# Performance work log

Measured on AMD Instinct MI355X. Metric: run time of the kernel, lower is better.

The kernel has to match this reference:

```python
import jax, jax.numpy as jnp
import numpy as np

NUM_LEVELS = 4
RADIUS = 4
H, W = 64, 128


def _bilinear_sample(feat, x, y):
    # feat: [N, Hl, Wl]; x, y: [N, K, K] pixel coords; zeros padding, align_corners=True
    N, Hl, Wl = feat.shape
    x0 = jnp.floor(x)
    y0 = jnp.floor(y)
    x1 = x0 + 1.0
    y1 = y0 + 1.0
    wx1 = x - x0
    wx0 = 1.0 - wx1
    wy1 = y - y0
    wy0 = 1.0 - wy1
    n_idx = jnp.arange(N)[:, None, None]

    def gather(xi, yi):
        inb = (xi >= 0) & (xi <= Wl - 1) & (yi >= 0) & (yi <= Hl - 1)
        xc = jnp.clip(xi, 0, Wl - 1).astype(jnp.int32)
        yc = jnp.clip(yi, 0, Hl - 1).astype(jnp.int32)
        v = feat[n_idx, yc, xc]
        return jnp.where(inb, v, jnp.zeros((), feat.dtype))

    return (gather(x0, y0) * wx0 * wy0 + gather(x1, y0) * wx1 * wy0
            + gather(x0, y1) * wx0 * wy1 + gather(x1, y1) * wx1 * wy1)


def _correlation(fmap1, fmap2, coords):
    bs, dim, h, w = fmap1.shape
    f1 = fmap1.reshape(bs, dim, h * w)
    f2 = fmap2.reshape(bs, dim, h * w)
    cv = jnp.einsum('bdm,bdn->bmn', f1, f2) / jnp.sqrt(jnp.asarray(dim, jnp.float32))
    cv = cv.reshape(bs * h * w, h, w)
    pyramid = [cv]
    for _ in range(NUM_LEVELS - 1):
        N, hl, wl = cv.shape
        cv = cv.reshape(N, hl // 2, 2, wl // 2, 2).mean(axis=(2, 4))  # avg_pool2d(2,2)
        pyramid.append(cv)

    cxy = coords.transpose(0, 2, 3, 1).astype(jnp.float32)  # [bs,h,w,2]
    cx = cxy[..., 0].reshape(-1)  # [bs*h*w]
    cy = cxy[..., 1].reshape(-1)
    r = RADIUS
    d = jnp.linspace(-r, r, 2 * r + 1, dtype=jnp.float32)
    dy, dx = jnp.meshgrid(d, d, indexing='ij')  # [K,K]

    outs = []
    for i, corr in enumerate(pyramid):
        scale = jnp.float32(2 ** i)
        x = cx[:, None, None] / scale + dx[None]
        y = cy[:, None, None] / scale + dy[None]
        sampled = _bilinear_sample(corr, x, y)  # [bs*h*w, K, K]
        outs.append(sampled.reshape(bs, h, w, -1))
    out = jnp.concatenate(outs, axis=-1)  # [bs,h,w,num_levels*K*K]
    return out.transpose(0, 3, 1, 2)


def setup_inputs() -> dict:
    key = jax.random.key(0)
    k1, k2, k3, k4 = jax.random.split(key, 4)
    fmap1 = jax.random.normal(k1, (1, 256, H, W), dtype=jnp.float32)
    fmap2 = jax.random.normal(k2, (1, 256, H, W), dtype=jnp.float32)
    cx = jax.random.uniform(k3, (1, 1, H, W), dtype=jnp.float32) * (W - 1)
    cy = jax.random.uniform(k4, (1, 1, H, W), dtype=jnp.float32) * (H - 1)
    coords = jnp.concatenate([cx, cy], axis=1)  # [1,2,H,W], channel 0 = x, 1 = y
    return {"fmap1": fmap1, "fmap2": fmap2, "coords": coords}


def reference(fmap1, fmap2, coords):
    return _correlation(fmap1, fmap2, coords)
```

## Files before the change

kernel.cpp:

```cpp
#include <hip/hip_runtime.h>
#include <stdint.h>

typedef _Float16 f16;
typedef __attribute__((ext_vector_type(8))) _Float16 f16x8;
typedef __attribute__((ext_vector_type(4))) float f32x4;
typedef __attribute__((ext_vector_type(2))) float fv2;
typedef __attribute__((ext_vector_type(4))) float fv4;

#define H0 64
#define W0 128
#define NPIX 8192
#define KD 256
#define NCAT 10880
#define OFF1 8192
#define OFF2 10240
#define OFF3 10752
#define CAP0 640
#define CAP1 2048
#define PL1OFF (32 * CAP0)
#define PLTOT (PL1OFF + 8 * CAP1)
#define ZTOT (64 + PLTOT + 64)


__global__ __launch_bounds__(256) void fused_pre(const float* __restrict__ in0,
                                                 const float* __restrict__ in1,
                                                 const float* __restrict__ coords,
                                                 f16* __restrict__ At,
                                                 f16* __restrict__ Bt,
                                                 int2* __restrict__ meta,
                                                 int* __restrict__ cnt) {
  __shared__ f16 tile[64][65];
  __shared__ int hist[40];
  __shared__ int base[40];
  int bid = blockIdx.x;
  int t = threadIdx.x;

  if (bid < 1024) {
    const float* in = (bid < 512) ? in0 : in1;
    f16* out = (bid < 512) ? At : Bt;
    size_t NR = (bid < 512) ? NPIX : NCAT;
    int bx = bid & 511;
    int m0 = (bx & 127) * 64;
    int d0 = (bx >> 7) * 64;
    int a = t & 63, b = t >> 6;
#pragma unroll
    for (int i = 0; i < 16; ++i) {
      int d = b + i * 4;
      tile[a][d] = (f16)in[(size_t)(d0 + d) * NPIX + m0 + a];
    }
    __syncthreads();
#pragma unroll
    for (int i = 0; i < 16; ++i) {
      int m = b + i * 4;
      int d = d0 + a;
      out[((size_t)(d >> 5) * NR + (m0 + m)) * 32 + (d & 31)] = tile[m][a];
    }
  } else if (bid < 1360) {
    int idx = (bid - 1024) * 256 + t;
    float acc[8] = {0, 0, 0, 0, 0, 0, 0, 0};
    int r, dc;
    if (idx < 65536) {
      int r1 = idx & 2047; dc = idx >> 11; r = r1;
      int y = r1 >> 6, x = r1 & 63;
#pragma unroll
      for (int e = 0; e < 8; ++e) {
        const float* p = in1 + (size_t)(dc * 8 + e) * NPIX + (y * 2) * W0 + x * 2;
        fv2 s0 = *(const fv2*)p;
        fv2 s1 = *(const fv2*)(p + W0);
        acc[e] = (s0[0] + s0[1] + s1[0] + s1[1]) * 0.25f;
      }
    } else if (idx < 81920) {
      int i2 = idx - 65536;
      int r2 = i2 & 511; dc = i2 >> 9; r = 2048 + r2;
      int y = r2 >> 5, x = r2 & 31;
#pragma unroll
      for (int e = 0; e < 8; ++e) {
        const float* p = in1 + (size_t)(dc * 8 + e) * NPIX + (y * 4) * W0 + x * 4;
        float s = 0.f;
#pragma unroll
        for (int h = 0; h < 4; ++h) {
          fv4 v = *(const fv4*)(p + h * W0);
          s += v[0] + v[1] + v[2] + v[3];
        }
        acc[e] = s * 0.0625f;
      }
    } else {
      int i3 = idx - 81920;
      int r3 = i3 & 127; dc = i3 >> 7; r = 2560 + r3;
      int y = r3 >> 4, x = r3 & 15;
#pragma unroll
      for (int e = 0; e < 8; ++e) {
        const float* p = in1 + (size_t)(dc * 8 + e) * NPIX + (y * 8) * W0 + x * 8;
        float s = 0.f;
#pragma unroll
        for (int h = 0; h < 8; ++h) {
          fv4 v0 = *(const fv4*)(p + h * W0);
          fv4 v1 = *(const fv4*)(p + h * W0 + 4);
          s += v0[0] + v0[1] + v0[2] + v0[3] + v1[0] + v1[1] + v1[2] + v1[3];
        }
        acc[e] = s * 0.015625f;
      }
    }
    f16x8 o;
#pragma unroll
    for (int e = 0; e < 8; ++e) o[e] = (f16)acc[e];
    *(f16x8*)(Bt + ((size_t)(dc >> 2) * NCAT + 8192 + r) * 32 + (dc & 3) * 8) = o;
  } else {
    int* plist = cnt + 64;
    int m = (bid - 1360) * 256 + t;
    if (t < 40) hist[t] = 0;
    __syncthreads();

    float cx = coords[m];
    float cy = coords[NPIX + m];
    int X0l[2], Y0l[2];
    int mx = 0, my = 0;
#pragma unroll
    for (int lev = 0; lev < 4; ++lev) {
      float inv = 1.0f / (float)(1 << lev);
      int X0 = (int)floorf(cx * inv) - 4;
      int Y0 = (int)floorf(cy * inv) - 4;
      if (lev < 2) { X0l[lev] = X0; Y0l[lev] = Y0; }
      mx |= (X0 & 0xff) << (8 * lev);
      my |= (Y0 & 0xff) << (8 * lev);
    }
    meta[m] = make_int2(mx, my);

    int b0 = (min(max(Y0l[0], 0), 63) >> 4) * 8 + (min(max(X0l[0], 0), 127) >> 4);
    int b1 = (min(max(Y0l[1], 0), 31) >> 4) * 4 + (min(max(X0l[1], 0), 63) >> 4);
    int s0 = atomicAdd(&hist[b0], 1);
    int s1 = atomicAdd(&hist[32 + b1], 1);
    __syncthreads();

    if (t < 40) base[t] = atomicAdd(&cnt[t], hist[t]);
    __syncthreads();

    int p0 = base[b0] + s0;
    if (p0 < CAP0) plist[b0 * CAP0 + p0] = m;
    int p1 = base[32 + b1] + s1;
    if (p1 < CAP1) plist[PL1OFF + b1 * CAP1 + p1] = m;
  }
}

__global__ __launch_bounds__(256, 2) void gemm_all(const f16* __restrict__ At,
                                                   const f16* __restrict__ Bt,
                                                   const int* __restrict__ cnt,
                                                   const int2* __restrict__ meta,
                                                   f16* __restrict__ Wbuf) {
  __shared__ f16 sa[8192];
  const int* plist = cnt + 64;
  int bid = blockIdx.x;
  int t = threadIdx.x;
  int lane = t & 63;
  int w = t >> 6;
  int lr = lane & 15;
  int ko = lane >> 4;

  if (bid < 160) {
    int bm = (((bid & 7) << 2) | ((bid >> 3) & 3)) << 8;
    int bn = OFF2 + ((bid >> 5) << 7);

    const f16* Ab = At + (size_t)(bm + w * 64 + lr) * 32 + ko * 8;
    const f16* Bb = Bt + (size_t)(bn + lr) * 32 + ko * 8;

    f16x8 af[2][4], bf[2][8];
#define LOADK(s, kk)                                                           \
    do {                                                                       \
      const f16* ap = Ab + (size_t)(kk) * (NPIX * 32);                         \
      const f16* bp = Bb + (size_t)(kk) * (NCAT * 32);                         \
      _Pragma("unroll")                                                        \
      for (int i = 0; i < 4; ++i) af[s][i] = *(const f16x8*)(ap + i * 512);    \
      _Pragma("unroll")                                                        \
      for (int i = 0; i < 8; ++i) bf[s][i] = *(const f16x8*)(bp + i * 512);    \
    } while (0)

    f32x4 acc[4][8];
#pragma unroll
    for (int i = 0; i < 4; ++i)
#pragma unroll
      for (int j = 0; j < 8; ++j) acc[i][j] = (f32x4){0.f, 0.f, 0.f, 0.f};

    LOADK(0, 0);
    LOADK(1, 1);
#pragma unroll
    for (int kk = 0; kk < 8; ++kk) {
      const int cur = kk & 1;
#pragma unroll
      for (int mi = 0; mi < 4; ++mi)
#pragma unroll
        for (int ni = 0; ni < 8; ++ni)
          acc[mi][ni] = __builtin_amdgcn_mfma_f32_16x16x32_f16(
              af[cur][mi], bf[cur][ni], acc[mi][ni], 0, 0, 0);
      if (kk + 2 < 8) LOADK(cur, kk + 2);
    }
#undef LOADK

    int lev, n0, wlog;
    if (bn < OFF3) { lev = 2; n0 = bn - OFF2; wlog = 5; }
    else           { lev = 3; n0 = bn - OFF3; wlog = 4; }
    int wmask = (1 << wlog) - 1;
    int yA = n0 >> wlog;
    int yB = (n0 + 127) >> wlog;
    int ycol[8], xcol[8];
#pragma unroll
    for (int ni = 0; ni < 8; ++ni) {
      int n = n0 + ni * 16 + lr;
      ycol[ni] = n >> wlog;
      xcol[ni] = n & wmask;
    }
    int sh = lev * 8;
#pragma unroll
    for (int mi = 0; mi < 4; ++mi)
#pragma unroll
      for (int r2 = 0; r2 < 4; ++r2) {
        int grow = bm + w * 64 + mi * 16 + ko * 4 + r2;
        int2 mv = meta[grow];
        int Y0 = (int)(signed char)((mv.y >> sh) & 0xff);
        if (Y0 <= yB && Y0 + 9 >= yA) {
          int X0 = (int)(signed char)((mv.x >> sh) & 0xff);
          f16* rowp = Wbuf + (size_t)grow * 512 + lev * 128;
#pragma unroll
          for (int ni = 0; ni < 8; ++ni) {
            int dy = ycol[ni] - Y0;
            int dx = xcol[ni] - X0;
            if ((unsigned)dy < 10u && (unsigned)dx < 10u)
              rowp[dy * 12 + dx] = (f16)(acc[mi][ni][r2] * 0.0625f);
          }
        }
      }
    return;
  }

  int bb = bid - 160;
  int lev, b, mg, half;
  if (bb < 1280) { lev = 0; b = bb / 40; int r = bb % 40; mg = r >> 1; half = r & 1; }
  else { lev = 1; int i = bb - 1280; b = i / 128; int r = i % 128; mg = r >> 1; half = r & 1; }

  int CAP   = lev ? CAP1 : CAP0;
  int cb    = min(cnt[lev ? 32 + b : b], CAP);
  if (mg * 32 >= cb) return;
  int Hl    = lev ? 32 : 64;
  int Wmap  = lev ? 64 : 128;
  int bx    = lev ? (b & 3) : (b & 7);
  int by    = lev ? (b >> 2) : (b >> 3);
  int x0 = bx * 16, y0 = by * 16;
  int NY = min(25, Hl - y0);
  int rowbase = lev ? 8192 : 0;
  int pbase = (lev ? PL1OFF + b * CAP1 : b * CAP0) + mg * 32;

  {
    int spix = t >> 3;
    int skk  = t & 7;
    int sp = plist[pbase + spix] & (NPIX - 1);
    const f16* g = At + (size_t)skk * (NPIX * 32) + (size_t)sp * 32;
    int line = spix >> 1;
    int sb = (spix & 1) * 4;
    f16* dst = sa + skk * 1024 + line * 64;
#pragma unroll
    for (int q = 0; q < 4; ++q) {
      int phys = (sb + q) ^ (line & 7) ^ skk;
      *(f16x8*)(dst + phys * 8) = *(const f16x8*)(g + q * 8);
    }
  }

  int aoff[2];
#pragma unroll
  for (int mi = 0; mi < 2; ++mi) {
    int pl = mi * 16 + lr;
    int line = pl >> 1;
    int phys = ((pl & 1) * 4 + ko) ^ (line & 7);
    aoff[mi] = line * 64 + phys * 8;
  }

  bool vst[4];
  int brow[4];
#pragma unroll
  for (int st = 0; st < 4; ++st) {
    int q = w + 4 * st;
    int yl = half * 13 + q;
    vst[st] = (q < (half ? 12 : 13)) && (yl < NY);
    int ylc = min(yl, NY - 1);
    brow[st] = rowbase + (y0 + ylc) * Wmap + x0 + lr;
  }

  f16x8 bf[2][8];
#define BLDB(s_, kk_)                                                          \
  do {                                                                         \
    const f16* bp = Bt + (size_t)(kk_) * (NCAT * 32) + ko * 8;                 \
    _Pragma("unroll")                                                          \
    for (int st = 0; st < 4; ++st) {                                           \
      bf[s_][st * 2]     = *(const f16x8*)(bp + (size_t)brow[st] * 32);        \
      bf[s_][st * 2 + 1] = *(const f16x8*)(bp + (size_t)(brow[st] + 16) * 32); \
    }                                                                          \
  } while (0)

  BLDB(0, 0);
  BLDB(1, 1);

  f32x4 acc[8][2];
#pragma unroll
  for (int i = 0; i < 8; ++i)
#pragma unroll
    for (int j = 0; j < 2; ++j) acc[i][j] = (f32x4){0.f, 0.f, 0.f, 0.f};

  __syncthreads();

#pragma unroll
  for (int kk = 0; kk < 8; ++kk) {
    const int cur = kk & 1;
    f16x8 a0 = *(const f16x8*)(sa + kk * 1024 + (aoff[0] ^ (kk * 8)));
    f16x8 a1 = *(const f16x8*)(sa + kk * 1024 + (aoff[1] ^ (kk * 8)));
#pragma unroll
    for (int nf = 0; nf < 8; ++nf) {
      acc[nf][0] = __builtin_amdgcn_mfma_f32_16x16x32_f16(a0, bf[cur][nf],
                                                          acc[nf][0], 0, 0, 0);
      acc[nf][1] = __builtin_amdgcn_mfma_f32_16x16x32_f16(a1, bf[cur][nf],
                                                          acc[nf][1], 0, 0, 0);
    }
    if (kk + 2 < 8) BLDB(cur, kk + 2);
  }
#undef BLDB

  int pe[2][4];
  int Xp[2][4], Yp[2][4];
  int sh = lev * 8;
#pragma unroll
  for (int mi = 0; mi < 2; ++mi)
#pragma unroll
    for (int r2 = 0; r2 < 4; ++r2) {
      int slot = mg * 32 + mi * 16 + ko * 4 + r2;
      int p = plist[pbase + mi * 16 + ko * 4 + r2] & (NPIX - 1);
      pe[mi][r2] = (slot < cb) ? p : -1;
      int2 mv = meta[p];
      Xp[mi][r2] = (int)(signed char)((mv.x >> sh) & 0xff);
      Yp[mi][r2] = (int)(signed char)((mv.y >> sh) & 0xff);
    }
#pragma unroll
  for (int st = 0; st < 4; ++st) {
    if (!vst[st]) continue;
    int y = y0 + half * 13 + w + 4 * st;
#pragma unroll
    for (int xc = 0; xc < 2; ++xc) {
      int x = x0 + xc * 16 + lr;
#pragma unroll
      for (int mi = 0; mi < 2; ++mi)
#pragma unroll
        for (int r2 = 0; r2 < 4; ++r2) {
          int p = pe[mi][r2];
          int dy = y - Yp[mi][r2];
          int dx = x - Xp[mi][r2];
          if (p >= 0 && (unsigned)dy < 10u && (unsigned)dx < 10u)
            Wbuf[(size_t)p * 512 + lev * 128 + dy * 12 + dx] =
                (f16)(acc[st * 2 + xc][mi][r2] * 0.0625f);
        }
    }
  }
}

__global__ __launch_bounds__(64) void corr_sample(const f16* __restrict__ Wbuf,
                                                  const float* __restrict__ coords,
                                                  float* __restrict__ out) {
  int tid = blockIdx.x * 64 + threadIdx.x;
  int m = tid & (NPIX - 1);
  int lev = tid >> 13;
  int Hl = H0 >> lev, Wl = W0 >> lev;

  float cx = coords[m];
  float cy = coords[NPIX + m];
  float inv = 1.0f / (float)(1 << lev);
  float xb = cx * inv, yb = cy * inv;
  float fx = floorf(xb), fy = floorf(yb);
  int X0 = (int)fx - 4, Y0 = (int)fy - 4;
  float wx1 = xb - fx, wx0 = 1.0f - wx1;
  float wy1 = yb - fy, wy0 = 1.0f - wy1;

  const f16* wb = Wbuf + (size_t)m * 512 + lev * 128;
  f16x8 rv[15];
#pragma unroll
  for (int i = 0; i < 15; ++i) rv[i] = *(const f16x8*)(wb + i * 8);

  float* op = out + (size_t)lev * 81 * NPIX + m;
  float cur[11], nxt[11];
#pragma unroll
  for (int i = 0; i < 11; ++i) {
    bool in = ((unsigned)Y0 < (unsigned)Hl) && ((unsigned)(X0 + i) < (unsigned)Wl);
    cur[i] = in ? (float)rv[i >> 3][i & 7] : 0.0f;
  }
#pragma unroll
  for (int j = 0; j < 9; ++j) {
    bool yin = (unsigned)(Y0 + j + 1) < (unsigned)Hl;
#pragma unroll
    for (int i = 0; i < 11; ++i) {
      int c = (j + 1) * 12 + i;
      bool in = yin && ((unsigned)(X0 + i) < (unsigned)Wl);
      nxt[i] = in ? (float)rv[c >> 3][c & 7] : 0.0f;
    }
#pragma unroll
    for (int i = 0; i < 9; ++i) {
      float v = wy0 * (wx0 * cur[i] + wx1 * cur[i + 1])
              + wy1 * (wx0 * nxt[i] + wx1 * nxt[i + 1]);
      op[(size_t)(j * 9 + i) * NPIX] = v;
    }
#pragma unroll
    for (int i = 0; i < 11; ++i) cur[i] = nxt[i];
  }
}

extern "C" void kernel_launch(void* const* d_in, const int* in_sizes, int n_in,
                              void* d_out, int out_size, void* d_ws, size_t ws_size,
                              hipStream_t stream) {
  const float* fmap1  = (const float*)d_in[0];
  const float* fmap2  = (const float*)d_in[1];
  const float* coords = (const float*)d_in[2];
  float* out = (float*)d_out;

  char* ws = (char*)d_ws;
  size_t offA = 0;
  size_t offB = offA + (size_t)NPIX * KD * 2;
  size_t offW = offB + (size_t)NCAT * KD * 2;
  size_t offM = offW + (size_t)NPIX * 512 * 2;
  size_t offC = offM + (size_t)NPIX * 8;
  size_t need = offC + (size_t)ZTOT * 4;
  if (ws_size < need) return;

  f16*  At   = (f16*)(ws + offA);
  f16*  Bt   = (f16*)(ws + offB);
  f16*  Wbuf = (f16*)(ws + offW);
  int2* meta = (int2*)(ws + offM);
  int*  cnt  = (int*)(ws + offC);

  hipMemsetAsync(cnt, 0, 64 * sizeof(int), stream);
  fused_pre<<<1392, 256, 0, stream>>>(fmap1, fmap2, coords, At, Bt, meta, cnt);
  gemm_all<<<2464, 256, 0, stream>>>(At, Bt, cnt, meta, Wbuf);
  corr_sample<<<512, 64, 0, stream>>>(Wbuf, coords, out);
}
```

Before: 74.71 us.

## Split gemm_all into single-wave blocks with finer pixel and tile-fragment partitioning

Converts gemm_all from 256-thread blocks to 64-thread single-wavefront blocks. The dense part now gets one block per former wave, and the sparse level-0/1 part gets one block per 16-pixel group × 8-fragment chunk. The A operand is loaded straight from global into registers instead of staged through shared memory, and the barrier is gone. The aim is better load balance and finer early-exit on sparse bins. In exchange the grid grows to many more tiny blocks, A is no longer reused across waves, and per-block launch and metadata overhead go up.

Result: slower. 85.20 us (+14.0%).

```diff
diff --git a/kernel.cpp b/kernel.cpp
--- a/kernel.cpp
+++ b/kernel.cpp
@@ -142,23 +142,22 @@
   }
 }
 
-__global__ __launch_bounds__(256, 2) void gemm_all(const f16* __restrict__ At,
-                                                   const f16* __restrict__ Bt,
-                                                   const int* __restrict__ cnt,
-                                                   const int2* __restrict__ meta,
-                                                   f16* __restrict__ Wbuf) {
-  __shared__ f16 sa[8192];
+__global__ __launch_bounds__(64) void gemm_all(const f16* __restrict__ At,
+                                               const f16* __restrict__ Bt,
+                                               const int* __restrict__ cnt,
+                                               const int2* __restrict__ meta,
+                                               f16* __restrict__ Wbuf) {
   const int* plist = cnt + 64;
   int bid = blockIdx.x;
-  int t = threadIdx.x;
-  int lane = t & 63;
-  int w = t >> 6;
+  int lane = threadIdx.x;
   int lr = lane & 15;
   int ko = lane >> 4;
 
-  if (bid < 160) {
-    int bm = (((bid & 7) << 2) | ((bid >> 3) & 3)) << 8;
-    int bn = OFF2 + ((bid >> 5) << 7);
+  if (bid < 640) {
+    int obid = bid >> 2;
+    int w = bid & 3;
+    int bm = (((obid & 7) << 2) | ((obid >> 3) & 3)) << 8;
+    int bn = OFF2 + ((obid >> 5) << 7);
 
     const f16* Ab = At + (size_t)(bm + w * 64 + lr) * 32 + ko * 8;
     const f16* Bb = Bt + (size_t)(bn + lr) * 32 + ko * 8;
@@ -231,128 +230,86 @@
     return;
   }
 
-  int bb = bid - 160;
-  int lev, b, mg, half;
-  if (bb < 1280) { lev = 0; b = bb / 40; int r = bb % 40; mg = r >> 1; half = r & 1; }
-  else { lev = 1; int i = bb - 1280; b = i / 128; int r = i % 128; mg = r >> 1; half = r & 1; }
-
-  int CAP   = lev ? CAP1 : CAP0;
-  int cb    = min(cnt[lev ? 32 + b : b], CAP);
-  if (mg * 32 >= cb) return;
-  int Hl    = lev ? 32 : 64;
-  int Wmap  = lev ? 64 : 128;
-  int bx    = lev ? (b & 3) : (b & 7);
-  int by    = lev ? (b >> 2) : (b >> 3);
+  int u = bid - 640;
+  int lev, b, pg, fg;
+  if (u < 8960) { lev = 0; b = u / 280; int r = u % 280; pg = r / 7; fg = r % 7; }
+  else          { int v = u - 8960; lev = 1; b = v / 896; int r = v % 896; pg = r / 7; fg = r % 7; }
+
+  int CAP  = lev ? CAP1 : CAP0;
+  int cb   = min(cnt[lev ? 32 + b : b], CAP);
+  if (pg * 16 >= cb) return;
+  int Hl   = lev ? 32 : 64;
+  int Wmap = lev ? 64 : 128;
+  int bx   = lev ? (b & 3) : (b & 7);
+  int by   = lev ? (b >> 2) : (b >> 3);
   int x0 = bx * 16, y0 = by * 16;
   int NY = min(25, Hl - y0);
+  int NF = NY * 2;
+  int f0 = fg * 8;
+  if (f0 >= NF) return;
+  int FN = min(8, NF - f0);
   int rowbase = lev ? 8192 : 0;
-  int pbase = (lev ? PL1OFF + b * CAP1 : b * CAP0) + mg * 32;
-
-  {
-    int spix = t >> 3;
-    int skk  = t & 7;
-    int sp = plist[pbase + spix] & (NPIX - 1);
-    const f16* g = At + (size_t)skk * (NPIX * 32) + (size_t)sp * 32;
-    int line = spix >> 1;
-    int sb = (spix & 1) * 4;
-    f16* dst = sa + skk * 1024 + line * 64;
-#pragma unroll
-    for (int q = 0; q < 4; ++q) {
-      int phys = (sb + q) ^ (line & 7) ^ skk;
-      *(f16x8*)(dst + phys * 8) = *(const f16x8*)(g + q * 8);
-    }
-  }
-
-  int aoff[2];
-#pragma unroll
-  for (int mi = 0; mi < 2; ++mi) {
-    int pl = mi * 16 + lr;
-    int line = pl >> 1;
-    int phys = ((pl & 1) * 4 + ko) ^ (line & 7);
-    aoff[mi] = line * 64 + phys * 8;
-  }
-
-  bool vst[4];
-  int brow[4];
-#pragma unroll
-  for (int st = 0; st < 4; ++st) {
-    int q = w + 4 * st;
-    int yl = half * 13 + q;
-    vst[st] = (q < (half ? 12 : 13)) && (yl < NY);
-    int ylc = min(yl, NY - 1);
-    brow[st] = rowbase + (y0 + ylc) * Wmap + x0 + lr;
+  int pbase = (lev ? PL1OFF + b * CAP1 : b * CAP0) + pg * 16;
+
+  int myp = plist[pbase + lr] & (NPIX - 1);
+  f16x8 af[8];
+#pragma unroll
+  for (int kk = 0; kk < 8; ++kk)
+    af[kk] = *(const f16x8*)(At + (size_t)kk * (NPIX * 32) + (size_t)myp * 32 + ko * 8);
+
+  int pe_[4], Xp_[4], Yp_[4];
+  int sh = lev * 8;
+#pragma unroll
+  for (int r2 = 0; r2 < 4; ++r2) {
+    int slot = ko * 4 + r2;
+    int p = plist[pbase + slot] & (NPIX - 1);
+    pe_[r2] = (pg * 16 + slot < cb) ? p : -1;
+    int2 mv = meta[p];
+    Xp_[r2] = (int)(signed char)((mv.x >> sh) & 0xff);
+    Yp_[r2] = (int)(signed char)((mv.y >> sh) & 0xff);
   }
 
   f16x8 bf[2][8];
-#define BLDB(s_, kk_)                                                          \
+#define BFLOAD(buf, fi)                                                        \
   do {                                                                         \
-    const f16* bp = Bt + (size_t)(kk_) * (NCAT * 32) + ko * 8;                 \
+    int gf = f0 + (fi);                                                        \
+    int brow = rowbase + (y0 + (gf >> 1)) * Wmap + x0 + (gf & 1) * 16 + lr;    \
     _Pragma("unroll")                                                          \
-    for (int st = 0; st < 4; ++st) {                                           \
-      bf[s_][st * 2]     = *(const f16x8*)(bp + (size_t)brow[st] * 32);        \
-      bf[s_][st * 2 + 1] = *(const f16x8*)(bp + (size_t)(brow[st] + 16) * 32); \
-    }                                                                          \
+    for (int kk = 0; kk < 8; ++kk)                                             \
+      bf[buf][kk] = *(const f16x8*)(Bt + (size_t)kk * (NCAT * 32) +            \
+                                    (size_t)brow * 32 + ko * 8);               \
   } while (0)
 
-  BLDB(0, 0);
-  BLDB(1, 1);
-
-  f32x4 acc[8][2];
-#pragma unroll
-  for (int i = 0; i < 8; ++i)
-#pragma unroll
-    for (int j = 0; j < 2; ++j) acc[i][j] = (f32x4){0.f, 0.f, 0.f, 0.f};
-
-  __syncthreads();
-
-#pragma unroll
-  for (int kk = 0; kk < 8; ++kk) {
-    const int cur = kk & 1;
-    f16x8 a0 = *(const f16x8*)(sa + kk * 1024 + (aoff[0] ^ (kk * 8)));
-    f16x8 a1 = *(const f16x8*)(sa + kk * 1024 + (aoff[1] ^ (kk * 8)));
-#pragma unroll
-    for (int nf = 0; nf < 8; ++nf) {
-      acc[nf][0] = __builtin_amdgcn_mfma_f32_16x16x32_f16(a0, bf[cur][nf],
-                                                          acc[nf][0], 0, 0, 0);
-      acc[nf][1] = __builtin_amdgcn_mfma_f32_16x16x32_f16(a1, bf[cur][nf],
-                                                          acc[nf][1], 0, 0, 0);
-    }
-    if (kk + 2 < 8) BLDB(cur, kk + 2);
-  }
-#undef BLDB
-
-  int pe[2][4];
-  int Xp[2][4], Yp[2][4];
-  int sh = lev * 8;
-#pragma unroll
-  for (int mi = 0; mi < 2; ++mi)
+  f32x4 acc[8];
+#pragma unroll
+  for (int i = 0; i < 8; ++i) acc[i] = (f32x4){0.f, 0.f, 0.f, 0.f};
+
+  BFLOAD(0, 0);
+#pragma unroll
+  for (int f = 0; f < 8; ++f) {
+    if (f >= FN) break;
+    if (f + 1 < FN) BFLOAD((f + 1) & 1, f + 1);
+#pragma unroll
+    for (int kk = 0; kk < 8; ++kk)
+      acc[f] = __builtin_amdgcn_mfma_f32_16x16x32_f16(af[kk], bf[f & 1][kk],
+                                                      acc[f], 0, 0, 0);
+  }
+#undef BFLOAD
+
+#pragma unroll
+  for (int f = 0; f < 8; ++f) {
+    if (f >= FN) break;
+    int gf = f0 + f;
+    int y = y0 + (gf >> 1);
+    int x = x0 + (gf & 1) * 16 + lr;
 #pragma unroll
     for (int r2 = 0; r2 < 4; ++r2) {
-      int slot = mg * 32 + mi * 16 + ko * 4 + r2;
-      int p = plist[pbase + mi * 16 + ko * 4 + r2] & (NPIX - 1);
-      pe[mi][r2] = (slot < cb) ? p : -1;
-      int2 mv = meta[p];
-      Xp[mi][r2] = (int)(signed char)((mv.x >> sh) & 0xff);
-      Yp[mi][r2] = (int)(signed char)((mv.y >> sh) & 0xff);
-    }
-#pragma unroll
-  for (int st = 0; st < 4; ++st) {
-    if (!vst[st]) continue;
-    int y = y0 + half * 13 + w + 4 * st;
-#pragma unroll
-    for (int xc = 0; xc < 2; ++xc) {
-      int x = x0 + xc * 16 + lr;
-#pragma unroll
-      for (int mi = 0; mi < 2; ++mi)
-#pragma unroll
-        for (int r2 = 0; r2 < 4; ++r2) {
-          int p = pe[mi][r2];
-          int dy = y - Yp[mi][r2];
-          int dx = x - Xp[mi][r2];
-          if (p >= 0 && (unsigned)dy < 10u && (unsigned)dx < 10u)
-            Wbuf[(size_t)p * 512 + lev * 128 + dy * 12 + dx] =
-                (f16)(acc[st * 2 + xc][mi][r2] * 0.0625f);
-        }
+      int p = pe_[r2];
+      int dy = y - Yp_[r2];
+      int dx = x - Xp_[r2];
+      if (p >= 0 && (unsigned)dy < 10u && (unsigned)dx < 10u)
+        Wbuf[(size_t)p * 512 + lev * 128 + dy * 12 + dx] =
+            (f16)(acc[f][r2] * 0.0625f);
     }
   }
 }
@@ -431,6 +388,6 @@
 
   hipMemsetAsync(cnt, 0, 64 * sizeof(int), stream);
   fused_pre<<<1392, 256, 0, stream>>>(fmap1, fmap2, coords, At, Bt, meta, cnt);
-  gemm_all<<<2464, 256, 0, stream>>>(At, Bt, cnt, meta, Wbuf);
+  gemm_all<<<16768, 64, 0, stream>>>(At, Bt, cnt, meta, Wbuf);
   corr_sample<<<512, 64, 0, stream>>>(Wbuf, coords, out);
 }
```
